# Performance work log

Measured on AMD Instinct MI355X. Metric: run time of the kernel, lower is better.

The kernel has to match this reference:

```python
import jax, jax.numpy as jnp
import numpy as np

D_MODEL = 1024
NUM_HEADS = 16
HEAD_DIM = D_MODEL // NUM_HEADS
BATCH, SEQ = 2, 2048


def setup_inputs() -> dict:
    key = jax.random.key(0)
    k1, k2, k3, k4, k5 = jax.random.split(key, 5)
    x = jax.random.normal(k1, (BATCH, SEQ, D_MODEL), dtype=jnp.float32)
    mask = jnp.ones((BATCH, SEQ), dtype=jnp.int32)
    s = 1.0 / np.sqrt(D_MODEL)
    W_qkv = jax.random.uniform(k2, (D_MODEL, 3 * D_MODEL), jnp.float32, -s, s)
    b_qkv = jax.random.uniform(k3, (3 * D_MODEL,), jnp.float32, -s, s)
    W_proj = jax.random.uniform(k4, (D_MODEL, D_MODEL), jnp.float32, -s, s)
    b_proj = jax.random.uniform(k5, (D_MODEL,), jnp.float32, -s, s)
    return {"x": x, "mask": mask, "W_qkv": W_qkv, "b_qkv": b_qkv,
            "W_proj": W_proj, "b_proj": b_proj}


def reference(x, mask, W_qkv, b_qkv, W_proj, b_proj):
    B, S, _ = x.shape
    qkv = x @ W_qkv + b_qkv                                  # [B,S,3D]
    q, k, v = jnp.split(qkv, 3, axis=-1)
    def heads(t):  # [B,S,D] -> [B,H,S,hd]
        return t.reshape(B, S, NUM_HEADS, HEAD_DIM).transpose(0, 2, 1, 3)
    q, k, v = heads(q), heads(k), heads(v)
    scores = jnp.einsum('bhqd,bhkd->bhqk', q, k) / np.sqrt(HEAD_DIM)
    # mask: [B,S] key-padding -> [B,1,1,S], positions where mask==0 get -inf
    scores = jnp.where(mask[:, None, None, :] == 0, -jnp.inf, scores)
    attn = jax.nn.softmax(scores, axis=-1)
    ctx = jnp.einsum('bhqk,bhkd->bhqd', attn, v)             # [B,H,S,hd]
    ctx = ctx.transpose(0, 2, 1, 3).reshape(B, S, D_MODEL)
    return ctx @ W_proj + b_proj
```

## Files before the change

kernel.cpp:

```cpp
#include <hip/hip_runtime.h>


#define BATCH 2
#define SEQ 2048
#define DMODEL 1024
#define NHEADS 16
#define HDIM 64
#define BS (BATCH * SEQ)
#define N3 (3 * DMODEL)
#define QSCALE 0.18033688011112042f

typedef float f32x4 __attribute__((ext_vector_type(4)));
typedef float f32x16 __attribute__((ext_vector_type(16)));
typedef short bf16x8 __attribute__((ext_vector_type(8)));
typedef unsigned short u16;
typedef unsigned short u16x4 __attribute__((ext_vector_type(4)));

typedef const __attribute__((address_space(1))) unsigned int* gptr_t;
typedef __attribute__((address_space(3))) unsigned int* sptr_t;

__device__ __forceinline__ u16 f2bf(float f) {
  unsigned int u = __float_as_uint(f);
  return (u16)((u + 0x7fffu + ((u >> 16) & 1u)) >> 16);
}

__device__ __forceinline__ void gload_lds16(const void* g, void* l) {
  __builtin_amdgcn_global_load_lds((gptr_t)g, (sptr_t)l, 16, 0, 0);
}

__device__ __forceinline__ unsigned cvtpk(float lo, float hi) {
  unsigned r;
  asm("v_cvt_pk_bf16_f32 %0, %1, %2" : "=v"(r) : "v"(lo), "v"(hi));
  return r;
}

__device__ __forceinline__ void pl32swap(unsigned& d, unsigned& s) {
  asm volatile("v_permlane32_swap_b32 %0, %1" : "+v"(d), "+v"(s));
}

#define WAIT_VM4() asm volatile("s_waitcnt vmcnt(4)" ::: "memory")
#define WAIT_VM0() asm volatile("s_waitcnt vmcnt(0)" ::: "memory")

__global__ __launch_bounds__(256) void conv_x(const float* __restrict__ in,
                                              u16* __restrict__ out, int n4) {
  int i = blockIdx.x * 256 + threadIdx.x;
  if (i >= n4) return;
  float4 v = ((const float4*)in)[i];
  u16x4 o;
  o[0] = f2bf(v.x); o[1] = f2bf(v.y); o[2] = f2bf(v.z); o[3] = f2bf(v.w);
  ((u16x4*)out)[i] = o;
}

__global__ __launch_bounds__(256) void transp(const float* __restrict__ in,
                                              u16* __restrict__ out, int R, int C) {
  __shared__ float tile[64][65];
  int tx = threadIdx.x & 63, ty = threadIdx.x >> 6;
  int c0 = blockIdx.x * 64, r0 = blockIdx.y * 64;
#pragma unroll
  for (int j = ty; j < 64; j += 4)
    tile[j][tx] = in[(size_t)(r0 + j) * C + c0 + tx];
  __syncthreads();
#pragma unroll
  for (int j = ty; j < 64; j += 4)
    out[(size_t)(c0 + j) * R + r0 + tx] = f2bf(tile[tx][j]);
}

template <int MODE>
__global__ __launch_bounds__(256) void gemm_bt(
    const u16* __restrict__ A, const u16* __restrict__ Bt,
    const float* __restrict__ bias, float* __restrict__ outf,
    u16* __restrict__ qkb, u16* __restrict__ vtb, int M, int N, int K) {
  __shared__ __align__(16) u16 lds[3 * 2 * 4096];
  const int nwgx = gridDim.x;
  const int nwg = nwgx * gridDim.y;
  const int idx = blockIdx.y * nwgx + blockIdx.x;
  const int swz = (idx & 7) * (nwg >> 3) + (idx >> 3);
  const int m0 = (swz / nwgx) * 128, n0 = (swz % nwgx) * 128;

  const int tid = threadIdx.x;
  const int lane = tid & 63, w = tid >> 6;
  const int wr = w >> 1, wc = w & 1;
  const int lg = lane >> 4, lr = lane & 15;
  const int NK = K >> 5;

  f32x4 acc[4][4] = {};

  const int srow = tid >> 2;
  const int scb = (tid & 3) << 4;
  const char* Abase = (const char*)A + ((size_t)(m0 + srow) * K) * 2 + scb;
  const char* Bbase = (const char*)Bt + ((size_t)(n0 + srow) * K) * 2 + scb;
  const size_t half = (size_t)64 * K * 2;

  auto stage = [&](int buf, int kk) {
    char* dst = (char*)lds + buf * 16384;
    const char* a = Abase + kk * 64;
    gload_lds16(a, dst + tid * 16);
    gload_lds16(a + half, dst + 4096 + tid * 16);
    const char* b = Bbase + kk * 64;
    gload_lds16(b, dst + 8192 + tid * 16);
    gload_lds16(b + half, dst + 12288 + tid * 16);
  };

  stage(0, 0);
  stage(1, 1);
  int bi = 0;
  for (int kk = 0; kk < NK; ++kk) {
    if (kk < NK - 1) WAIT_VM4(); else WAIT_VM0();
    __builtin_amdgcn_s_barrier();
    if (kk + 2 < NK) stage(bi == 0 ? 2 : bi - 1, kk + 2);
    const u16* lA = lds + bi * 8192;
    const u16* lB = lA + 4096;
    bf16x8 af[4], bfr[4];
#pragma unroll
    for (int i = 0; i < 4; ++i)
      af[i] = *(const bf16x8*)(lA + (wr * 64 + i * 16 + lr) * 32 + lg * 8);
#pragma unroll
    for (int j = 0; j < 4; ++j)
      bfr[j] = *(const bf16x8*)(lB + (wc * 64 + j * 16 + lr) * 32 + lg * 8);
#pragma unroll
    for (int i = 0; i < 4; ++i)
#pragma unroll
      for (int j = 0; j < 4; ++j)
        acc[i][j] = __builtin_amdgcn_mfma_f32_16x16x32_bf16(af[i], bfr[j],
                                                            acc[i][j], 0, 0, 0);
    bi = (bi == 2) ? 0 : bi + 1;
  }

#pragma unroll
  for (int i = 0; i < 4; ++i) {
    const int rowb = m0 + wr * 64 + i * 16 + lg * 4;
#pragma unroll
    for (int j = 0; j < 4; ++j) {
      const int col = n0 + wc * 64 + j * 16 + lr;
      const float bv = bias[col];
      if (MODE == 0) {
        if (col < 2 * DMODEL) {
          const float qs = (col < DMODEL) ? QSCALE : 1.0f;
#pragma unroll
          for (int r = 0; r < 4; ++r)
            qkb[(size_t)(rowb + r) * (2 * DMODEL) + col] =
                f2bf((acc[i][j][r] + bv) * qs);
        } else {
          const int hd = col - 2 * DMODEL;
          const int b = rowb >> 11, s0 = rowb & (SEQ - 1);
          u16x4 pk;
#pragma unroll
          for (int r = 0; r < 4; ++r) pk[r] = f2bf(acc[i][j][r] + bv);
          *(u16x4*)(vtb +
                    ((size_t)((b * NHEADS + (hd >> 6)) * HDIM + (hd & 63))) * SEQ +
                    s0) = pk;
        }
      } else {
#pragma unroll
        for (int r = 0; r < 4; ++r)
          outf[(size_t)(rowb + r) * N + col] = acc[i][j][r] + bv;
      }
    }
  }
}

__global__ __launch_bounds__(256) void attn(const u16* __restrict__ qkb,
                                            const u16* __restrict__ vtb,
                                            const int* __restrict__ mask,
                                            u16* __restrict__ ctxb) {
  __shared__ __align__(16) u16 Kl[3][64 * 64];
  __shared__ __align__(16) u16 Vl[4][64 * 64];

  const int idx = (blockIdx.z * gridDim.y + blockIdx.y) * gridDim.x + blockIdx.x;
  const int swz = (idx & 7) * 64 + (idx >> 3);
  const int q0 = (swz & 15) * 128;
  const int h = (swz >> 4) & 15;
  const int b = swz >> 8;

  const int tid = threadIdx.x;
  const int lane = tid & 63, w = tid >> 6;
  const int qi = lane & 31;
  const int hi = lane >> 5;
  const int q = q0 + w * 32 + qi;

  bool anyz;
  {
    const int4* mrow = (const int4*)(mask + b * SEQ);
    int z = 0;
#pragma unroll
    for (int p = 0; p < 8; ++p) {
      int4 m = mrow[lane + p * 64];
      z |= (m.x == 0) | (m.y == 0) | (m.z == 0) | (m.w == 0);
    }
    anyz = __any(z);
  }

  bf16x8 qreg[4];
  {
    const u16* Qrow = qkb + (size_t)(b * SEQ + q) * (2 * DMODEL) + h * HDIM;
#pragma unroll
    for (int kc = 0; kc < 4; ++kc)
      qreg[kc] = *(const bf16x8*)(Qrow + kc * 16 + hi * 8);
  }

  float m_run = -3.0e38f, l_run = 0.f;
  f32x16 ct0 = (f32x16)0.f, ct1 = (f32x16)0.f;

  const u16* Kg = qkb + (size_t)(b * SEQ) * (2 * DMODEL) + DMODEL + h * HDIM;
  const u16* Vg = vtb + (size_t)((b * NHEADS + h) * HDIM) * SEQ;
  const int srow = tid >> 3;
  const int scol = ((tid & 7) ^ (srow & 7)) << 4;

  auto stage = [&](int t) {
    const int kb = t % 3, vb = t & 3;
    const int k0 = t * 64;
    const char* ks = (const char*)(Kg + (size_t)(k0 + srow) * (2 * DMODEL)) + scol;
    gload_lds16(ks, (char*)Kl[kb] + tid * 16);
    gload_lds16(ks + (size_t)32 * (2 * DMODEL) * 2,
                (char*)Kl[kb] + 4096 + tid * 16);
    const char* vs = (const char*)(Vg + (size_t)srow * SEQ + k0) + scol;
    gload_lds16(vs, (char*)Vl[vb] + tid * 16);
    gload_lds16(vs + (size_t)32 * SEQ * 2, (char*)Vl[vb] + 4096 + tid * 16);
  };

  auto qkt = [&](int t, f32x16& s0, f32x16& s1) {
    const char* Kb = (const char*)Kl[t % 3];
    __builtin_amdgcn_s_setprio(1);
#pragma unroll
    for (int kc = 0; kc < 4; ++kc) {
      const int sl = (((kc << 1) | hi) ^ (lane & 7)) << 4;
      bf16x8 kf0 = *(const bf16x8*)(Kb + qi * 128 + sl);
      bf16x8 kf1 = *(const bf16x8*)(Kb + (32 + qi) * 128 + sl);
      s0 = __builtin_amdgcn_mfma_f32_32x32x16_bf16(kf0, qreg[kc], s0, 0, 0, 0);
      s1 = __builtin_amdgcn_mfma_f32_32x32x16_bf16(kf1, qreg[kc], s1, 0, 0, 0);
    }
    __builtin_amdgcn_s_setprio(0);
  };

  auto pv = [&](int t, const unsigned pk[16]) {
    const char* Vb = (const char*)Vl[t & 3];
    __builtin_amdgcn_s_setprio(1);
#pragma unroll
    for (int ks = 0; ks < 4; ++ks) {
      const int mb = (ks >> 1) * 8 + (ks & 1) * 4;
      unsigned b0 = pk[mb + 0], b2 = pk[mb + 2];
      unsigned b1 = pk[mb + 1], b3 = pk[mb + 3];
      pl32swap(b0, b2);
      pl32swap(b1, b3);
      union { unsigned u[4]; bf16x8 v; } bu;
      bu.u[0] = b0; bu.u[1] = b1; bu.u[2] = b2; bu.u[3] = b3;
      const int sl = (((ks << 1) | hi) ^ (lane & 7)) << 4;
      bf16x8 vf0 = *(const bf16x8*)(Vb + qi * 128 + sl);
      bf16x8 vf1 = *(const bf16x8*)(Vb + (32 + qi) * 128 + sl);
      ct0 = __builtin_amdgcn_mfma_f32_32x32x16_bf16(vf0, bu.v, ct0, 0, 0, 0);
      ct1 = __builtin_amdgcn_mfma_f32_32x32x16_bf16(vf1, bu.v, ct1, 0, 0, 0);
    }
    __builtin_amdgcn_s_setprio(0);
  };

  auto softmax = [&](f32x16& s0, f32x16& s1, int t, bool use_mask,
                     unsigned pk[16]) {
    if (use_mask) {
      const int base = b * SEQ + t * 64;
#pragma unroll
      for (int r = 0; r < 16; ++r) {
        const int key = (r & 3) + 8 * (r >> 2) + 4 * hi;
        if (mask[base + key] == 0) s0[r] = -3.0e38f;
        if (mask[base + 32 + key] == 0) s1[r] = -3.0e38f;
      }
    }
    float pm = fmaxf(fmaxf(s0[0], s0[1]), s0[2]);
#pragma unroll
    for (int r = 3; r < 16; r += 2) pm = fmaxf(fmaxf(pm, s0[r]), s0[r + 1]);
#pragma unroll
    for (int r = 0; r < 16; r += 2) pm = fmaxf(fmaxf(pm, s1[r]), s1[r + 1]);
    pm = fmaxf(pm, __shfl_xor(pm, 32));
    if (__any(pm > m_run + 8.f)) {
      const float mn = fmaxf(m_run, pm);
      const float corr = __builtin_amdgcn_exp2f(m_run - mn);
      m_run = mn;
      l_run *= corr;
#pragma unroll
      for (int r = 0; r < 16; ++r) { ct0[r] *= corr; ct1[r] *= corr; }
    }
    float ls = 0.f;
#pragma unroll
    for (int r = 0; r < 16; ++r) {
      s0[r] = __builtin_amdgcn_exp2f(s0[r] - m_run); ls += s0[r];
    }
#pragma unroll
    for (int r = 0; r < 16; ++r) {
      s1[r] = __builtin_amdgcn_exp2f(s1[r] - m_run); ls += s1[r];
    }
    l_run += ls + __shfl_xor(ls, 32);
#pragma unroll
    for (int rp = 0; rp < 8; ++rp) {
      pk[rp] = cvtpk(s0[2 * rp], s0[2 * rp + 1]);
      pk[8 + rp] = cvtpk(s1[2 * rp], s1[2 * rp + 1]);
    }
  };

  const int NT = SEQ / 64;
  unsigned pkp[16];
  stage(0);
  stage(1);
  if (!anyz) {
    WAIT_VM4();
    __builtin_amdgcn_s_barrier();
    stage(2);
    {
      f32x16 s0 = (f32x16)0.f, s1 = (f32x16)0.f;
      qkt(0, s0, s1);
      softmax(s0, s1, 0, false, pkp);
    }
    for (int t = 1; t < NT; ++t) {
      if (t < NT - 1) WAIT_VM4(); else WAIT_VM0();
      __builtin_amdgcn_s_barrier();
      if (t + 2 < NT) stage(t + 2);
      f32x16 s0 = (f32x16)0.f, s1 = (f32x16)0.f;
      qkt(t, s0, s1);
      pv(t - 1, pkp);
      softmax(s0, s1, t, false, pkp);
    }
    pv(NT - 1, pkp);
  } else {
    for (int t = 0; t < NT; ++t) {
      __syncthreads();
      if (t + 2 < NT) stage(t + 2);
      __syncthreads();
      f32x16 s0 = (f32x16)0.f, s1 = (f32x16)0.f;
      qkt(t, s0, s1);
      softmax(s0, s1, t, true, pkp);
      pv(t, pkp);
    }
  }

  const float rl = __builtin_amdgcn_rcpf(l_run);
  u16* orow = ctxb + (size_t)(b * SEQ + q) * DMODEL + h * HDIM;
#pragma unroll
  for (int g = 0; g < 4; ++g) {
    {
      const int d0 = 8 * g + 4 * hi;
      uint2 st;
      st.x = cvtpk(ct0[4 * g] * rl, ct0[4 * g + 1] * rl);
      st.y = cvtpk(ct0[4 * g + 2] * rl, ct0[4 * g + 3] * rl);
      *(uint2*)(orow + d0) = st;
    }
    {
      const int d0 = 32 + 8 * g + 4 * hi;
      uint2 st;
      st.x = cvtpk(ct1[4 * g] * rl, ct1[4 * g + 1] * rl);
      st.y = cvtpk(ct1[4 * g + 2] * rl, ct1[4 * g + 3] * rl);
      *(uint2*)(orow + d0) = st;
    }
  }
}

extern "C" void kernel_launch(void* const* d_in, const int* in_sizes, int n_in,
                              void* d_out, int out_size, void* d_ws, size_t ws_size,
                              hipStream_t stream) {
  const float* x = (const float*)d_in[0];
  const int* mask = (const int*)d_in[1];
  const float* Wqkv = (const float*)d_in[2];
  const float* bqkv = (const float*)d_in[3];
  const float* Wproj = (const float*)d_in[4];
  const float* bproj = (const float*)d_in[5];
  float* out = (float*)d_out;

  char* ws = (char*)d_ws;
  u16* xb = (u16*)(ws);
  u16* wqkvt = (u16*)(ws + 8388608);
  u16* wprojt = (u16*)(ws + 14680064);
  u16* qkb = (u16*)(ws + 16777216);
  u16* vtb = (u16*)(ws + 33554432);
  u16* ctxb = (u16*)(ws + 41943040);

  conv_x<<<dim3((BS * DMODEL / 4 + 255) / 256), 256, 0, stream>>>(x, xb,
                                                                  BS * DMODEL / 4);
  transp<<<dim3(N3 / 64, DMODEL / 64), 256, 0, stream>>>(Wqkv, wqkvt, DMODEL, N3);
  transp<<<dim3(DMODEL / 64, DMODEL / 64), 256, 0, stream>>>(Wproj, wprojt, DMODEL,
                                                             DMODEL);
  gemm_bt<0><<<dim3(N3 / 128, BS / 128), 256, 0, stream>>>(
      xb, wqkvt, bqkv, nullptr, qkb, vtb, BS, N3, DMODEL);
  attn<<<dim3(SEQ / 128, NHEADS, BATCH), 256, 0, stream>>>(qkb, vtb, mask, ctxb);
  gemm_bt<1><<<dim3(DMODEL / 128, BS / 128), 256, 0, stream>>>(
      ctxb, wprojt, bproj, out, nullptr, nullptr, BS, DMODEL, DMODEL);
}
```

Measured before the change: 199.2 us.

## Split attention over key halves and merge partial results in a combine kernel

Attention is split along the key dimension into two halves, doubling the grid from 512 to 1024 blocks. Each block writes unnormalised fp32 partial context plus its running max and sum, and a new combine kernel rescales and merges the halves into bf16 context. The inner loop also drops the software pipelining that overlapped QK^T of one tile with PV of the previous tile, and uses a simpler double buffer with an extra barrier per tile. This trades more fp32 global traffic and an extra launch for more parallelism across the GPU's compute units.

```diff
diff --git a/kernel.cpp b/kernel.cpp
--- a/kernel.cpp
+++ b/kernel.cpp
@@ -162,15 +162,18 @@
 __global__ __launch_bounds__(256) void attn(const u16* __restrict__ qkb,
                                             const u16* __restrict__ vtb,
                                             const int* __restrict__ mask,
-                                            u16* __restrict__ ctxb) {
-  __shared__ __align__(16) u16 Kl[3][64 * 64];
-  __shared__ __align__(16) u16 Vl[4][64 * 64];
+                                            float* __restrict__ ctxp,
+                                            float* __restrict__ ml) {
+  __shared__ __align__(16) u16 Kl[2][64 * 64];
+  __shared__ __align__(16) u16 Vl[2][64 * 64];
 
   const int idx = (blockIdx.z * gridDim.y + blockIdx.y) * gridDim.x + blockIdx.x;
-  const int swz = (idx & 7) * 64 + (idx >> 3);
+  const int swz = (idx & 7) * 128 + (idx >> 3);
   const int q0 = (swz & 15) * 128;
   const int h = (swz >> 4) & 15;
-  const int b = swz >> 8;
+  const int bh = swz >> 8;
+  const int b = bh >> 1;
+  const int khalf = bh & 1;
 
   const int tid = threadIdx.x;
   const int lane = tid & 63, w = tid >> 6;
@@ -207,19 +210,21 @@
   const int scol = ((tid & 7) ^ (srow & 7)) << 4;
 
   auto stage = [&](int t) {
-    const int kb = t % 3, vb = t & 3;
+    const int buf = t & 1;
     const int k0 = t * 64;
     const char* ks = (const char*)(Kg + (size_t)(k0 + srow) * (2 * DMODEL)) + scol;
-    gload_lds16(ks, (char*)Kl[kb] + tid * 16);
+    gload_lds16(ks, (char*)Kl[buf] + tid * 16);
     gload_lds16(ks + (size_t)32 * (2 * DMODEL) * 2,
-                (char*)Kl[kb] + 4096 + tid * 16);
+                (char*)Kl[buf] + 4096 + tid * 16);
     const char* vs = (const char*)(Vg + (size_t)srow * SEQ + k0) + scol;
-    gload_lds16(vs, (char*)Vl[vb] + tid * 16);
-    gload_lds16(vs + (size_t)32 * SEQ * 2, (char*)Vl[vb] + 4096 + tid * 16);
+    gload_lds16(vs, (char*)Vl[buf] + tid * 16);
+    gload_lds16(vs + (size_t)32 * SEQ * 2, (char*)Vl[buf] + 4096 + tid * 16);
   };
 
-  auto qkt = [&](int t, f32x16& s0, f32x16& s1) {
-    const char* Kb = (const char*)Kl[t % 3];
+  auto compute = [&](int t, bool use_mask) {
+    const int buf = t & 1;
+    f32x16 s0 = (f32x16)0.f, s1 = (f32x16)0.f;
+    const char* Kb = (const char*)Kl[buf];
     __builtin_amdgcn_s_setprio(1);
 #pragma unroll
     for (int kc = 0; kc < 4; ++kc) {
@@ -230,10 +235,49 @@
       s1 = __builtin_amdgcn_mfma_f32_32x32x16_bf16(kf1, qreg[kc], s1, 0, 0, 0);
     }
     __builtin_amdgcn_s_setprio(0);
-  };
-
-  auto pv = [&](int t, const unsigned pk[16]) {
-    const char* Vb = (const char*)Vl[t & 3];
+
+    if (use_mask) {
+      const int base = b * SEQ + t * 64;
+#pragma unroll
+      for (int r = 0; r < 16; ++r) {
+        const int key = (r & 3) + 8 * (r >> 2) + 4 * hi;
+        if (mask[base + key] == 0) s0[r] = -3.0e38f;
+        if (mask[base + 32 + key] == 0) s1[r] = -3.0e38f;
+      }
+    }
+
+    float pm = fmaxf(fmaxf(s0[0], s0[1]), s0[2]);
+#pragma unroll
+    for (int r = 3; r < 16; r += 2) pm = fmaxf(fmaxf(pm, s0[r]), s0[r + 1]);
+#pragma unroll
+    for (int r = 0; r < 16; r += 2) pm = fmaxf(fmaxf(pm, s1[r]), s1[r + 1]);
+    pm = fmaxf(pm, __shfl_xor(pm, 32));
+    if (__any(pm > m_run + 8.f)) {
+      const float mn = fmaxf(m_run, pm);
+      const float corr = __builtin_amdgcn_exp2f(m_run - mn);
+      m_run = mn;
+      l_run *= corr;
+#pragma unroll
+      for (int r = 0; r < 16; ++r) { ct0[r] *= corr; ct1[r] *= corr; }
+    }
+    float ls = 0.f;
+#pragma unroll
+    for (int r = 0; r < 16; ++r) {
+      s0[r] = __builtin_amdgcn_exp2f(s0[r] - m_run); ls += s0[r];
+    }
+#pragma unroll
+    for (int r = 0; r < 16; ++r) {
+      s1[r] = __builtin_amdgcn_exp2f(s1[r] - m_run); ls += s1[r];
+    }
+    l_run += ls + __shfl_xor(ls, 32);
+
+    unsigned pk[16];
+#pragma unroll
+    for (int rp = 0; rp < 8; ++rp) {
+      pk[rp] = cvtpk(s0[2 * rp], s0[2 * rp + 1]);
+      pk[8 + rp] = cvtpk(s1[2 * rp], s1[2 * rp + 1]);
+    }
+    const char* Vb = (const char*)Vl[buf];
     __builtin_amdgcn_s_setprio(1);
 #pragma unroll
     for (int ks = 0; ks < 4; ++ks) {
@@ -253,102 +297,73 @@
     __builtin_amdgcn_s_setprio(0);
   };
 
-  auto softmax = [&](f32x16& s0, f32x16& s1, int t, bool use_mask,
-                     unsigned pk[16]) {
-    if (use_mask) {
-      const int base = b * SEQ + t * 64;
-#pragma unroll
-      for (int r = 0; r < 16; ++r) {
-        const int key = (r & 3) + 8 * (r >> 2) + 4 * hi;
-        if (mask[base + key] == 0) s0[r] = -3.0e38f;
-        if (mask[base + 32 + key] == 0) s1[r] = -3.0e38f;
-      }
-    }
-    float pm = fmaxf(fmaxf(s0[0], s0[1]), s0[2]);
-#pragma unroll
-    for (int r = 3; r < 16; r += 2) pm = fmaxf(fmaxf(pm, s0[r]), s0[r + 1]);
-#pragma unroll
-    for (int r = 0; r < 16; r += 2) pm = fmaxf(fmaxf(pm, s1[r]), s1[r + 1]);
-    pm = fmaxf(pm, __shfl_xor(pm, 32));
-    if (__any(pm > m_run + 8.f)) {
-      const float mn = fmaxf(m_run, pm);
-      const float corr = __builtin_amdgcn_exp2f(m_run - mn);
-      m_run = mn;
-      l_run *= corr;
-#pragma unroll
-      for (int r = 0; r < 16; ++r) { ct0[r] *= corr; ct1[r] *= corr; }
-    }
-    float ls = 0.f;
-#pragma unroll
-    for (int r = 0; r < 16; ++r) {
-      s0[r] = __builtin_amdgcn_exp2f(s0[r] - m_run); ls += s0[r];
-    }
-#pragma unroll
-    for (int r = 0; r < 16; ++r) {
-      s1[r] = __builtin_amdgcn_exp2f(s1[r] - m_run); ls += s1[r];
-    }
-    l_run += ls + __shfl_xor(ls, 32);
-#pragma unroll
-    for (int rp = 0; rp < 8; ++rp) {
-      pk[rp] = cvtpk(s0[2 * rp], s0[2 * rp + 1]);
-      pk[8 + rp] = cvtpk(s1[2 * rp], s1[2 * rp + 1]);
-    }
-  };
-
-  const int NT = SEQ / 64;
-  unsigned pkp[16];
-  stage(0);
-  stage(1);
+  const int t0 = khalf * 16, tend = t0 + 16;
+  stage(t0);
   if (!anyz) {
-    WAIT_VM4();
-    __builtin_amdgcn_s_barrier();
-    stage(2);
-    {
-      f32x16 s0 = (f32x16)0.f, s1 = (f32x16)0.f;
-      qkt(0, s0, s1);
-      softmax(s0, s1, 0, false, pkp);
-    }
-    for (int t = 1; t < NT; ++t) {
-      if (t < NT - 1) WAIT_VM4(); else WAIT_VM0();
+    for (int t = t0; t < tend; ++t) {
+      if (t + 1 < tend) { stage(t + 1); WAIT_VM4(); } else { WAIT_VM0(); }
       __builtin_amdgcn_s_barrier();
-      if (t + 2 < NT) stage(t + 2);
-      f32x16 s0 = (f32x16)0.f, s1 = (f32x16)0.f;
-      qkt(t, s0, s1);
-      pv(t - 1, pkp);
-      softmax(s0, s1, t, false, pkp);
-    }
-    pv(NT - 1, pkp);
+      compute(t, false);
+      __builtin_amdgcn_s_barrier();
+    }
   } else {
-    for (int t = 0; t < NT; ++t) {
+    for (int t = t0; t < tend; ++t) {
       __syncthreads();
-      if (t + 2 < NT) stage(t + 2);
+      if (t + 1 < tend) stage(t + 1);
       __syncthreads();
-      f32x16 s0 = (f32x16)0.f, s1 = (f32x16)0.f;
-      qkt(t, s0, s1);
-      softmax(s0, s1, t, true, pkp);
-      pv(t, pkp);
-    }
-  }
-
-  const float rl = __builtin_amdgcn_rcpf(l_run);
-  u16* orow = ctxb + (size_t)(b * SEQ + q) * DMODEL + h * HDIM;
+      compute(t, true);
+    }
+  }
+
+  float* orow = ctxp + ((size_t)(khalf * BS + b * SEQ + q)) * DMODEL + h * HDIM;
 #pragma unroll
   for (int g = 0; g < 4; ++g) {
     {
-      const int d0 = 8 * g + 4 * hi;
-      uint2 st;
-      st.x = cvtpk(ct0[4 * g] * rl, ct0[4 * g + 1] * rl);
-      st.y = cvtpk(ct0[4 * g + 2] * rl, ct0[4 * g + 3] * rl);
-      *(uint2*)(orow + d0) = st;
+      float4 st = make_float4(ct0[4 * g], ct0[4 * g + 1], ct0[4 * g + 2],
+                              ct0[4 * g + 3]);
+      *(float4*)(orow + 8 * g + 4 * hi) = st;
     }
     {
-      const int d0 = 32 + 8 * g + 4 * hi;
-      uint2 st;
-      st.x = cvtpk(ct1[4 * g] * rl, ct1[4 * g + 1] * rl);
-      st.y = cvtpk(ct1[4 * g + 2] * rl, ct1[4 * g + 3] * rl);
-      *(uint2*)(orow + d0) = st;
-    }
-  }
+      float4 st = make_float4(ct1[4 * g], ct1[4 * g + 1], ct1[4 * g + 2],
+                              ct1[4 * g + 3]);
+      *(float4*)(orow + 32 + 8 * g + 4 * hi) = st;
+    }
+  }
+  if (hi == 0) {
+    float* mlp = ml + ((size_t)(khalf * BS + b * SEQ + q) * NHEADS + h) * 2;
+    mlp[0] = m_run;
+    mlp[1] = l_run;
+  }
+}
+
+__global__ __launch_bounds__(256) void combine(const float* __restrict__ ctxp,
+                                               const float* __restrict__ ml,
+                                               u16* __restrict__ ctxb) {
+  const int gid = blockIdx.x * 256 + threadIdx.x;
+  const int token = gid >> 7;
+  const int d0 = (gid & 127) << 3;
+  const int h = d0 >> 6;
+  const float2 ml0 = *(const float2*)(ml + ((size_t)token * NHEADS + h) * 2);
+  const float2 ml1 =
+      *(const float2*)(ml + ((size_t)(BS + token) * NHEADS + h) * 2);
+  const float M = fmaxf(ml0.x, ml1.x);
+  const float w0 = exp2f(ml0.x - M), w1 = exp2f(ml1.x - M);
+  const float rl = __builtin_amdgcn_rcpf(ml0.y * w0 + ml1.y * w1);
+  const float4* c0 = (const float4*)(ctxp + (size_t)token * DMODEL + d0);
+  const float4* c1 =
+      (const float4*)(ctxp + ((size_t)BS + token) * DMODEL + d0);
+  uint4 st;
+  {
+    float4 a = c0[0], v = c1[0];
+    st.x = cvtpk((a.x * w0 + v.x * w1) * rl, (a.y * w0 + v.y * w1) * rl);
+    st.y = cvtpk((a.z * w0 + v.z * w1) * rl, (a.w * w0 + v.w * w1) * rl);
+  }
+  {
+    float4 a = c0[1], v = c1[1];
+    st.z = cvtpk((a.x * w0 + v.x * w1) * rl, (a.y * w0 + v.y * w1) * rl);
+    st.w = cvtpk((a.z * w0 + v.z * w1) * rl, (a.w * w0 + v.w * w1) * rl);
+  }
+  *(uint4*)(ctxb + (size_t)token * DMODEL + d0) = st;
 }
 
 extern "C" void kernel_launch(void* const* d_in, const int* in_sizes, int n_in,
@@ -369,6 +384,8 @@
   u16* qkb = (u16*)(ws + 16777216);
   u16* vtb = (u16*)(ws + 33554432);
   u16* ctxb = (u16*)(ws + 41943040);
+  float* ctxp = (float*)(ws + 50331648);
+  float* ml = (float*)(ws + 83886080);
 
   conv_x<<<dim3((BS * DMODEL / 4 + 255) / 256), 256, 0, stream>>>(x, xb,
                                                                   BS * DMODEL / 4);
@@ -377,7 +394,9 @@
                                                              DMODEL);
   gemm_bt<0><<<dim3(N3 / 128, BS / 128), 256, 0, stream>>>(
       xb, wqkvt, bqkv, nullptr, qkb, vtb, BS, N3, DMODEL);
-  attn<<<dim3(SEQ / 128, NHEADS, BATCH), 256, 0, stream>>>(qkb, vtb, mask, ctxb);
+  attn<<<dim3(SEQ / 128, NHEADS, BATCH * 2), 256, 0, stream>>>(qkb, vtb, mask,
+                                                               ctxp, ml);
+  combine<<<dim3(BS * DMODEL / 8 / 256), 256, 0, stream>>>(ctxp, ml, ctxb);
   gemm_bt<1><<<dim3(DMODEL / 128, BS / 128), 256, 0, stream>>>(
       ctxb, wprojt, bproj, out, nullptr, nullptr, BS, DMODEL, DMODEL);
 }
```

Measured after the change: 216.0 us. 8.4% more time.
